# Kernel tuning notes

Measured on AMD Instinct MI355X. Metric: run time of the kernel, lower is better.

Reference implementation:

```python
import jax, jax.numpy as jnp
import numpy as np

D = 1024
H = 16
HD = D // H
FF = 4 * D
EPS = 1e-5


def setup_inputs() -> dict:
    key = jax.random.key(0)
    ks = jax.random.split(key, 16)
    s = lambda k, shape, scale: jax.random.normal(k, shape, dtype=jnp.float32) * scale
    inp = {
        "x": s(ks[0], (8, 1024, D), 1.0),
        "Wq": s(ks[1], (D, D), D ** -0.5), "bq": jnp.zeros((D,), jnp.float32),
        "Wk": s(ks[2], (D, D), D ** -0.5), "bk": jnp.zeros((D,), jnp.float32),
        "Wv": s(ks[3], (D, D), D ** -0.5), "bv": jnp.zeros((D,), jnp.float32),
        "Wo": s(ks[4], (D, D), D ** -0.5), "bo": jnp.zeros((D,), jnp.float32),
        "W1": s(ks[5], (D, FF), D ** -0.5), "b1": jnp.zeros((FF,), jnp.float32),
        "W2": s(ks[6], (FF, D), FF ** -0.5), "b2": jnp.zeros((D,), jnp.float32),
        "g1": jnp.ones((D,), jnp.float32), "be1": jnp.zeros((D,), jnp.float32),
        "g2": jnp.ones((D,), jnp.float32), "be2": jnp.zeros((D,), jnp.float32),
    }
    return inp


def _layernorm(x, g, b):
    mu = jnp.mean(x, axis=-1, keepdims=True)
    var = jnp.var(x, axis=-1, keepdims=True)
    return (x - mu) * jax.lax.rsqrt(var + EPS) * g + b


def reference(x, Wq, bq, Wk, bk, Wv, bv, Wo, bo, W1, b1, W2, b2, g1, be1, g2, be2):
    B, S, _ = x.shape
    # --- pre-norm attention block (dropout = identity in eval) ---
    h = _layernorm(x, g1, be1)
    q = (h @ Wq + bq).reshape(B, S, H, HD)
    k = (h @ Wk + bk).reshape(B, S, H, HD)
    v = (h @ Wv + bv).reshape(B, S, H, HD)
    scores = jnp.einsum('bqhd,bkhd->bhqk', q, k) / jnp.sqrt(jnp.float32(HD))
    attn = jax.nn.softmax(scores, axis=-1)
    ctx = jnp.einsum('bhqk,bkhd->bqhd', attn, v).reshape(B, S, D)
    x = x + (ctx @ Wo + bo)
    # --- pre-norm FFN block ---
    h = _layernorm(x, g2, be2)
    h = jax.nn.gelu(h @ W1 + b1, approximate=False)
    x = x + (h @ W2 + b2)
    return x
```

## Files before the change

### kernel.cpp

```cpp
#include <hip/hip_runtime.h>
#include <hip/hip_bf16.h>
#include <math.h>
#include <stdint.h>

typedef unsigned short u16;
typedef unsigned int u32;
typedef __attribute__((ext_vector_type(8))) short short8;
typedef __attribute__((ext_vector_type(4))) float f32x4;

__device__ __forceinline__ float b2f(u16 u) {
  union { u32 i; float f; } v; v.i = ((u32)u) << 16; return v.f;
}
__device__ __forceinline__ u16 f2b(float f) {
  union { float f; u32 i; } v; v.f = f;
  return (u16)((v.i + 0x7FFFu + ((v.i >> 16) & 1u)) >> 16);
}

__device__ __forceinline__ void gload_lds16(const u16* g, u16* l) {
  __builtin_amdgcn_global_load_lds((const __attribute__((address_space(1))) void*)g,
                                   (__attribute__((address_space(3))) void*)l, 16, 0, 0);
}

__global__ __launch_bounds__(256) void transpose_k(const float* __restrict__ in,
                                                   u16* __restrict__ out, int K, int N) {
  __shared__ u16 tile[32][33];
  int n0 = blockIdx.x * 32, k0 = blockIdx.y * 32;
  int tx = threadIdx.x & 31, ty = threadIdx.x >> 5;
  #pragma unroll
  for (int i = ty; i < 32; i += 8)
    tile[i][tx] = f2b(in[(size_t)(k0 + i) * N + n0 + tx]);
  __syncthreads();
  #pragma unroll
  for (int i = ty; i < 32; i += 8)
    out[(size_t)(n0 + i) * K + k0 + tx] = tile[tx][i];
}

__global__ __launch_bounds__(256) void cat3_k(const float* __restrict__ a, const float* __restrict__ b,
                                              const float* __restrict__ c, float* __restrict__ o) {
  int i = blockIdx.x * 256 + threadIdx.x;
  o[i] = i < 1024 ? a[i] : (i < 2048 ? b[i - 1024] : c[i - 2048]);
}

__global__ __launch_bounds__(256) void vtrans_k(const u16* __restrict__ qkv, u16* __restrict__ vt) {
  __shared__ u16 tile[32][33];
  int bh = blockIdx.y, b = bh >> 4, h = bh & 15;
  int s0 = (blockIdx.x & 31) * 32, d0 = (blockIdx.x >> 5) * 32;
  int tx = threadIdx.x & 31, ty = threadIdx.x >> 5;
  #pragma unroll
  for (int i = ty; i < 32; i += 8)
    tile[i][tx] = qkv[(size_t)(b * 1024 + s0 + i) * 3072 + 2048 + h * 64 + d0 + tx];
  __syncthreads();
  #pragma unroll
  for (int i = ty; i < 32; i += 8)
    vt[(size_t)(bh * 64 + d0 + i) * 1024 + s0 + tx] = tile[tx][i];
}

template<int FP32IN>
__global__ __launch_bounds__(256) void ln_k(const void* __restrict__ xv, const float* __restrict__ g,
                                            const float* __restrict__ be, u16* __restrict__ out) {
  int row = blockIdx.x, t = threadIdx.x;
  float f0, f1, f2, f3;
  if (FP32IN) {
    const float* xr = (const float*)xv + (size_t)row * 1024;
    float4 x4 = *(const float4*)(xr + t * 4);
    f0 = x4.x; f1 = x4.y; f2 = x4.z; f3 = x4.w;
  } else {
    const u16* xr = (const u16*)xv + (size_t)row * 1024;
    ushort4 x4 = *(const ushort4*)(xr + t * 4);
    f0 = b2f(x4.x); f1 = b2f(x4.y); f2 = b2f(x4.z); f3 = b2f(x4.w);
  }
  float s = f0 + f1 + f2 + f3;
  float ss = f0 * f0 + f1 * f1 + f2 * f2 + f3 * f3;
  #pragma unroll
  for (int off = 32; off > 0; off >>= 1) { s += __shfl_down(s, off); ss += __shfl_down(ss, off); }
  __shared__ float sb[4], ssb[4];
  if ((t & 63) == 0) { sb[t >> 6] = s; ssb[t >> 6] = ss; }
  __syncthreads();
  s = sb[0] + sb[1] + sb[2] + sb[3];
  ss = ssb[0] + ssb[1] + ssb[2] + ssb[3];
  float mu = s * (1.0f / 1024.0f);
  float var = ss * (1.0f / 1024.0f) - mu * mu;
  float rstd = rsqrtf(var + 1e-5f);
  float4 gv = *(const float4*)(g + t * 4);
  float4 bv = *(const float4*)(be + t * 4);
  ushort4 o;
  o.x = f2b((f0 - mu) * rstd * gv.x + bv.x);
  o.y = f2b((f1 - mu) * rstd * gv.y + bv.y);
  o.z = f2b((f2 - mu) * rstd * gv.z + bv.z);
  o.w = f2b((f3 - mu) * rstd * gv.w + bv.w);
  *(ushort4*)(out + (size_t)row * 1024 + t * 4) = o;
}

template<int ACT, int RESID, int OUTF32>
__global__ __launch_bounds__(256) void gemm_k(const u16* __restrict__ A, const u16* __restrict__ Bt,
                                              const float* __restrict__ bias, const void* __restrict__ resid,
                                              void* __restrict__ Cv, int M, int N, int K, int ldc) {
  __shared__ u16 As[2][128 * 32];
  __shared__ u16 Bs[2][128 * 32];
  int Ny = N >> 7;
  int lin = blockIdx.y * 64 + blockIdx.x;
  int c8 = lin & 7, sblk = lin >> 3;
  int mq = sblk / Ny;
  int m0 = ((mq << 3) | c8) << 7;
  int n0 = (sblk - mq * Ny) << 7;
  int t = threadIdx.x;
  int wave = t >> 6, lane = t & 63, quad = lane >> 4, l16 = lane & 15;
  int wm = (wave >> 1) * 64, wn = (wave & 1) * 64;
  f32x4 acc[4][4] = {};
  int lr = lane >> 2;
  int lc = (lane & 3) ^ (lr & 3);
  const u16* Ab = A + (size_t)(m0 + wave * 16 + lr) * K + lc * 8;
  const u16* Bb = Bt + (size_t)(n0 + wave * 16 + lr) * K + lc * 8;
  const int lb = wave * 16 * 32;
  const int rdoff = (quad ^ (l16 & 3)) * 8;
  #pragma unroll
  for (int i = 0; i < 2; i++) {
    gload_lds16(Ab + (size_t)i * 64 * K, &As[0][lb + i * 64 * 32]);
    gload_lds16(Bb + (size_t)i * 64 * K, &Bs[0][lb + i * 64 * 32]);
  }
  const int niter = K >> 5;
  for (int c = 0; c < niter; c++) {
    int buf = c & 1;
    __syncthreads();
    if (c + 1 < niter) {
      int k1 = (c + 1) << 5;
      #pragma unroll
      for (int i = 0; i < 2; i++) {
        gload_lds16(Ab + k1 + (size_t)i * 64 * K, &As[buf ^ 1][lb + i * 64 * 32]);
        gload_lds16(Bb + k1 + (size_t)i * 64 * K, &Bs[buf ^ 1][lb + i * 64 * 32]);
      }
    }
    short8 a[4], b[4];
    #pragma unroll
    for (int i = 0; i < 4; i++)
      a[i] = *(const short8*)(&As[buf][(wm + i * 16 + l16) * 32 + rdoff]);
    #pragma unroll
    for (int j = 0; j < 4; j++)
      b[j] = *(const short8*)(&Bs[buf][(wn + j * 16 + l16) * 32 + rdoff]);
    #pragma unroll
    for (int i = 0; i < 4; i++)
      #pragma unroll
      for (int j = 0; j < 4; j++)
        acc[i][j] = __builtin_amdgcn_mfma_f32_16x16x32_bf16(a[i], b[j], acc[i][j], 0, 0, 0);
  }
  float bcol[4];
  #pragma unroll
  for (int j = 0; j < 4; j++) bcol[j] = bias[n0 + wn + j * 16 + l16];
  #pragma unroll
  for (int i = 0; i < 4; i++) {
    #pragma unroll
    for (int r = 0; r < 4; r++) {
      int row = m0 + wm + i * 16 + quad * 4 + r;
      #pragma unroll
      for (int j = 0; j < 4; j++) {
        int col = n0 + wn + j * 16 + l16;
        float v = acc[i][j][r] + bcol[j];
        if (ACT == 1) {
          float e = v * (2.3022082f + 0.1029431f * v * v);
          float tt = exp2f(fminf(e, 80.0f));
          v = v * tt / (tt + 1.0f);
        }
        if (RESID == 1) v += b2f(((const u16*)resid)[(size_t)row * N + col]);
        if (RESID == 2) v += ((const float*)resid)[(size_t)row * N + col];
        if (OUTF32) ((float*)Cv)[(size_t)row * ldc + col] = v;
        else        ((u16*)Cv)[(size_t)row * ldc + col] = f2b(v);
      }
    }
  }
}

__global__ __launch_bounds__(256) void attn_k(const u16* __restrict__ QKV, const u16* __restrict__ VT,
                                              u16* __restrict__ ctx) {
  int bh = blockIdx.x;
  int b = bh >> 4;
  int q0 = blockIdx.y * 64;
  int t = threadIdx.x, wave = t >> 6, lane = t & 63, quad = lane >> 4, l16 = lane & 15;
  __shared__ u16 Ks[2][64 * 64];
  __shared__ u16 Vs[2][64 * 64];
  __shared__ u16 Plds[4][16][72];
  const size_t base = ((size_t)b * 1024) * 3072 + (size_t)(bh & 15) * 64;
  const u16* Kbase = QKV + base + 1024;
  const u16* vtb = VT + (size_t)bh * 64 * 1024;
  int lrow = lane >> 3;
  int lchunk = (lane & 7) ^ (lrow & 7);
  int srow = wave * 16;
  short8 qa[2];
  #pragma unroll
  for (int kh = 0; kh < 2; kh++)
    qa[kh] = *(const short8*)(QKV + base + (size_t)(q0 + wave * 16 + l16) * 3072 + kh * 32 + quad * 8);
  #pragma unroll
  for (int half = 0; half < 2; half++) {
    int r8 = srow + half * 8;
    gload_lds16(Kbase + (size_t)(r8 + lrow) * 3072 + lchunk * 8, &Ks[0][r8 * 64]);
    gload_lds16(vtb + (size_t)(r8 + lrow) * 1024 + lchunk * 8, &Vs[0][r8 * 64]);
  }
  f32x4 o[4] = {};
  float l_acc[4] = {0.f, 0.f, 0.f, 0.f};
  for (int c = 0; c < 16; c++) {
    int buf = c & 1;
    __syncthreads();
    if (c < 15) {
      #pragma unroll
      for (int half = 0; half < 2; half++) {
        int r8 = srow + half * 8;
        gload_lds16(Kbase + (size_t)((c + 1) * 64 + r8 + lrow) * 3072 + lchunk * 8, &Ks[buf ^ 1][r8 * 64]);
        gload_lds16(vtb + (size_t)(r8 + lrow) * 1024 + (c + 1) * 64 + lchunk * 8, &Vs[buf ^ 1][r8 * 64]);
      }
    }
    f32x4 s[4] = {};
    #pragma unroll
    for (int kh = 0; kh < 2; kh++)
      #pragma unroll
      for (int j = 0; j < 4; j++) {
        int row = j * 16 + l16;
        int pc = (kh * 4 + quad) ^ (row & 7);
        short8 kb = *(const short8*)(&Ks[buf][row * 64 + pc * 8]);
        s[j] = __builtin_amdgcn_mfma_f32_16x16x32_bf16(qa[kh], kb, s[j], 0, 0, 0);
      }
    #pragma unroll
    for (int j = 0; j < 4; j++)
      #pragma unroll
      for (int r = 0; r < 4; r++) {
        float p = exp2f(s[j][r] * 0.18033688011112042f);
        l_acc[r] += p;
        Plds[wave][quad * 4 + r][j * 16 + l16] = f2b(p);
      }
    #pragma unroll
    for (int kh = 0; kh < 2; kh++) {
      short8 pa = *(const short8*)(&Plds[wave][l16][kh * 32 + quad * 8]);
      #pragma unroll
      for (int d4 = 0; d4 < 4; d4++) {
        int row = d4 * 16 + l16;
        int pc = (kh * 4 + quad) ^ (row & 7);
        short8 vb = *(const short8*)(&Vs[buf][row * 64 + pc * 8]);
        o[d4] = __builtin_amdgcn_mfma_f32_16x16x32_bf16(pa, vb, o[d4], 0, 0, 0);
      }
    }
  }
  #pragma unroll
  for (int off = 1; off < 16; off <<= 1)
    #pragma unroll
    for (int r = 0; r < 4; r++) l_acc[r] += __shfl_xor(l_acc[r], off);
  #pragma unroll
  for (int r = 0; r < 4; r++) {
    float inv = 1.0f / l_acc[r];
    size_t row = (size_t)b * 1024 + q0 + wave * 16 + quad * 4 + r;
    #pragma unroll
    for (int d4 = 0; d4 < 4; d4++) {
      int col = (bh & 15) * 64 + d4 * 16 + l16;
      ctx[row * 1024 + col] = f2b(o[d4][r] * inv);
    }
  }
}

extern "C" void kernel_launch(void* const* d_in, const int* in_sizes, int n_in,
                              void* d_out, int out_size, void* d_ws, size_t ws_size,
                              hipStream_t stream) {
  const float* x   = (const float*)d_in[0];
  const float* Wq  = (const float*)d_in[1];  const float* bq  = (const float*)d_in[2];
  const float* Wk  = (const float*)d_in[3];  const float* bk  = (const float*)d_in[4];
  const float* Wv  = (const float*)d_in[5];  const float* bv  = (const float*)d_in[6];
  const float* Wo  = (const float*)d_in[7];  const float* bo  = (const float*)d_in[8];
  const float* W1  = (const float*)d_in[9];  const float* b1  = (const float*)d_in[10];
  const float* W2  = (const float*)d_in[11]; const float* b2  = (const float*)d_in[12];
  const float* g1  = (const float*)d_in[13]; const float* be1 = (const float*)d_in[14];
  const float* g2  = (const float*)d_in[15]; const float* be2 = (const float*)d_in[16];

  char* ws = (char*)d_ws;
  const size_t MB = 1024 * 1024;
  u16* h1    = (u16*)(ws + 0 * MB);
  u16* qkv   = (u16*)(ws + 16 * MB);
  u16* x1    = (u16*)(ws + 16 * MB);
  u16* h2    = (u16*)(ws + 32 * MB);
  u16* W2T   = (u16*)(ws + 48 * MB);
  u16* WqkvT = (u16*)(ws + 64 * MB);
  u16* WoT   = (u16*)(ws + 70 * MB);
  u16* W1T   = (u16*)(ws + 72 * MB);
  float* bqkv = (float*)(ws + 80 * MB);
  u16* h3f   = (u16*)(ws + 80 * MB);
  u16* vt    = h1;
  u16* ctx   = (u16*)d_out;
  float* out = (float*)d_out;

  transpose_k<<<dim3(32, 32), 256, 0, stream>>>(Wq, WqkvT, 1024, 1024);
  transpose_k<<<dim3(32, 32), 256, 0, stream>>>(Wk, WqkvT + (size_t)1024 * 1024, 1024, 1024);
  transpose_k<<<dim3(32, 32), 256, 0, stream>>>(Wv, WqkvT + (size_t)2048 * 1024, 1024, 1024);
  transpose_k<<<dim3(32, 32), 256, 0, stream>>>(Wo, WoT, 1024, 1024);
  transpose_k<<<dim3(128, 32), 256, 0, stream>>>(W1, W1T, 1024, 4096);
  cat3_k<<<12, 256, 0, stream>>>(bq, bk, bv, bqkv);

  ln_k<1><<<8192, 256, 0, stream>>>(x, g1, be1, h1);

  gemm_k<0, 0, 0><<<dim3(64, 24), 256, 0, stream>>>(h1, WqkvT, bqkv, nullptr, qkv,
                                                    8192, 3072, 1024, 3072);

  vtrans_k<<<dim3(64, 128), 256, 0, stream>>>(qkv, vt);

  attn_k<<<dim3(128, 16), 256, 0, stream>>>(qkv, vt, ctx);

  gemm_k<0, 2, 0><<<dim3(64, 8), 256, 0, stream>>>(ctx, WoT, bo, x, x1,
                                                   8192, 1024, 1024, 1024);

  transpose_k<<<dim3(32, 128), 256, 0, stream>>>(W2, W2T, 4096, 1024);

  ln_k<0><<<8192, 256, 0, stream>>>(x1, g2, be2, h2);

  gemm_k<1, 0, 0><<<dim3(64, 32), 256, 0, stream>>>(h2, W1T, b1, nullptr, h3f,
                                                    8192, 4096, 1024, 4096);
  gemm_k<0, 1, 1><<<dim3(64, 8), 256, 0, stream>>>(h3f, W2T, b2, x1, out,
                                                   8192, 1024, 4096, 1024);

  (void)in_sizes; (void)n_in; (void)out_size; (void)ws_size;
}
```

Baseline: 545.1 us.

## Triple-buffer GEMM LDS tiles with two-stage prefetch and manual waitcnt barriers

Changes the GEMM main loop from double to triple buffering in LDS, prefetching two K-tiles ahead. It replaces __syncthreads with explicit vmcnt waits plus s_barrier, so loads for later tiles can stay in flight across the barrier. It also raises wave priority around the MFMA block. This costs 50% more LDS per block, which may reduce occupancy, and it relies on the manual waitcnt counts being correct.

```diff
diff --git a/kernel.cpp b/kernel.cpp
--- a/kernel.cpp
+++ b/kernel.cpp
@@ -95,8 +95,8 @@
 __global__ __launch_bounds__(256) void gemm_k(const u16* __restrict__ A, const u16* __restrict__ Bt,
                                               const float* __restrict__ bias, const void* __restrict__ resid,
                                               void* __restrict__ Cv, int M, int N, int K, int ldc) {
-  __shared__ u16 As[2][128 * 32];
-  __shared__ u16 Bs[2][128 * 32];
+  __shared__ u16 As[3][128 * 32];
+  __shared__ u16 Bs[3][128 * 32];
   int Ny = N >> 7;
   int lin = blockIdx.y * 64 + blockIdx.x;
   int c8 = lin & 7, sblk = lin >> 3;
@@ -113,21 +113,29 @@
   const u16* Bb = Bt + (size_t)(n0 + wave * 16 + lr) * K + lc * 8;
   const int lb = wave * 16 * 32;
   const int rdoff = (quad ^ (l16 & 3)) * 8;
+  const int niter = K >> 5;
   #pragma unroll
   for (int i = 0; i < 2; i++) {
     gload_lds16(Ab + (size_t)i * 64 * K, &As[0][lb + i * 64 * 32]);
     gload_lds16(Bb + (size_t)i * 64 * K, &Bs[0][lb + i * 64 * 32]);
   }
-  const int niter = K >> 5;
+  #pragma unroll
+  for (int i = 0; i < 2; i++) {
+    gload_lds16(Ab + 32 + (size_t)i * 64 * K, &As[1][lb + i * 64 * 32]);
+    gload_lds16(Bb + 32 + (size_t)i * 64 * K, &Bs[1][lb + i * 64 * 32]);
+  }
+  asm volatile("s_waitcnt vmcnt(4)" ::: "memory");
+  __builtin_amdgcn_s_barrier();
+  __builtin_amdgcn_sched_barrier(0);
+  int buf = 0;
   for (int c = 0; c < niter; c++) {
-    int buf = c & 1;
-    __syncthreads();
-    if (c + 1 < niter) {
-      int k1 = (c + 1) << 5;
+    if (c + 2 < niter) {
+      int k2 = (c + 2) << 5;
+      int wb = buf + 2; if (wb >= 3) wb -= 3;
       #pragma unroll
       for (int i = 0; i < 2; i++) {
-        gload_lds16(Ab + k1 + (size_t)i * 64 * K, &As[buf ^ 1][lb + i * 64 * 32]);
-        gload_lds16(Bb + k1 + (size_t)i * 64 * K, &Bs[buf ^ 1][lb + i * 64 * 32]);
+        gload_lds16(Ab + k2 + (size_t)i * 64 * K, &As[wb][lb + i * 64 * 32]);
+        gload_lds16(Bb + k2 + (size_t)i * 64 * K, &Bs[wb][lb + i * 64 * 32]);
       }
     }
     short8 a[4], b[4];
@@ -137,11 +145,23 @@
     #pragma unroll
     for (int j = 0; j < 4; j++)
       b[j] = *(const short8*)(&Bs[buf][(wn + j * 16 + l16) * 32 + rdoff]);
+    __builtin_amdgcn_s_setprio(1);
     #pragma unroll
     for (int i = 0; i < 4; i++)
       #pragma unroll
       for (int j = 0; j < 4; j++)
         acc[i][j] = __builtin_amdgcn_mfma_f32_16x16x32_bf16(a[i], b[j], acc[i][j], 0, 0, 0);
+    __builtin_amdgcn_s_setprio(0);
+    if (c + 2 < niter) {
+      asm volatile("s_waitcnt vmcnt(4)" ::: "memory");
+    } else if (c + 1 < niter) {
+      asm volatile("s_waitcnt vmcnt(0)" ::: "memory");
+    }
+    if (c + 1 < niter) {
+      __builtin_amdgcn_s_barrier();
+      __builtin_amdgcn_sched_barrier(0);
+    }
+    buf = (buf == 2) ? 0 : buf + 1;
   }
   float bcol[4];
   #pragma unroll
```

New measurement: 554.8 us. About the same (+1.8%).

## Rewrite GEMM as 128x256 tile, 8 waves, triple-buffered K=64 pipeline

Applied to the files above, without the earlier changes.

The GEMM kernel moves from a 128x128 tile with 4 waves and double-buffered K=32 stages to a 128x256 tile with 8 waves and triple-buffered K=64 stages. Global-to-LDS prefetch is interleaved with the MFMA phases and guarded by explicit barriers, waitcnts and setprio. The aim is to hide load latency, raise arithmetic intensity per block and cut synchronisation per unit of K. The costs are more LDS (about 144KB) and fewer blocks, so occupancy drops and tail imbalance grows.

```diff
diff --git a/kernel.cpp b/kernel.cpp
--- a/kernel.cpp
+++ b/kernel.cpp
@@ -20,6 +20,9 @@
   __builtin_amdgcn_global_load_lds((const __attribute__((address_space(1))) void*)g,
                                    (__attribute__((address_space(3))) void*)l, 16, 0, 0);
 }
+
+#define LD8(p) (*(const short8*)(p))
+#define MFMA_BF16 __builtin_amdgcn_mfma_f32_16x16x32_bf16
 
 __global__ __launch_bounds__(256) void transpose_k(const float* __restrict__ in,
                                                    u16* __restrict__ out, int K, int N) {
@@ -92,56 +95,149 @@
 }
 
 template<int ACT, int RESID, int OUTF32>
-__global__ __launch_bounds__(256) void gemm_k(const u16* __restrict__ A, const u16* __restrict__ Bt,
+__global__ __launch_bounds__(512) void gemm_k(const u16* __restrict__ A, const u16* __restrict__ Bt,
                                               const float* __restrict__ bias, const void* __restrict__ resid,
                                               void* __restrict__ Cv, int M, int N, int K, int ldc) {
-  __shared__ u16 As[2][128 * 32];
-  __shared__ u16 Bs[2][128 * 32];
-  int Ny = N >> 7;
+  __shared__ u16 As[3][128 * 64];
+  __shared__ u16 Bs[3][256 * 64];
+  int Ny = N >> 8;
   int lin = blockIdx.y * 64 + blockIdx.x;
   int c8 = lin & 7, sblk = lin >> 3;
   int mq = sblk / Ny;
   int m0 = ((mq << 3) | c8) << 7;
-  int n0 = (sblk - mq * Ny) << 7;
+  int n0 = (sblk - mq * Ny) << 8;
   int t = threadIdx.x;
   int wave = t >> 6, lane = t & 63, quad = lane >> 4, l16 = lane & 15;
-  int wm = (wave >> 1) * 64, wn = (wave & 1) * 64;
+  int wm = (wave >> 2) << 6;
+  int wn = (wave & 3) << 6;
   f32x4 acc[4][4] = {};
-  int lr = lane >> 2;
-  int lc = (lane & 3) ^ (lr & 3);
-  const u16* Ab = A + (size_t)(m0 + wave * 16 + lr) * K + lc * 8;
-  const u16* Bb = Bt + (size_t)(n0 + wave * 16 + lr) * K + lc * 8;
-  const int lb = wave * 16 * 32;
-  const int rdoff = (quad ^ (l16 & 3)) * 8;
-  #pragma unroll
-  for (int i = 0; i < 2; i++) {
-    gload_lds16(Ab + (size_t)i * 64 * K, &As[0][lb + i * 64 * 32]);
-    gload_lds16(Bb + (size_t)i * 64 * K, &Bs[0][lb + i * 64 * 32]);
-  }
-  const int niter = K >> 5;
-  for (int c = 0; c < niter; c++) {
-    int buf = c & 1;
-    __syncthreads();
-    if (c + 1 < niter) {
-      int k1 = (c + 1) << 5;
-      #pragma unroll
-      for (int i = 0; i < 2; i++) {
-        gload_lds16(Ab + k1 + (size_t)i * 64 * K, &As[buf ^ 1][lb + i * 64 * 32]);
-        gload_lds16(Bb + k1 + (size_t)i * 64 * K, &Bs[buf ^ 1][lb + i * 64 * 32]);
-      }
-    }
-    short8 a[4], b[4];
-    #pragma unroll
-    for (int i = 0; i < 4; i++)
-      a[i] = *(const short8*)(&As[buf][(wm + i * 16 + l16) * 32 + rdoff]);
-    #pragma unroll
-    for (int j = 0; j < 4; j++)
-      b[j] = *(const short8*)(&Bs[buf][(wn + j * 16 + l16) * 32 + rdoff]);
-    #pragma unroll
-    for (int i = 0; i < 4; i++)
-      #pragma unroll
-      for (int j = 0; j < 4; j++)
-        acc[i][j] = __builtin_amdgcn_mfma_f32_16x16x32_bf16(a[i], b[j], acc[i][j], 0, 0, 0);
+  int lrow = lane >> 3;
+  int lchunk = (lane & 7) ^ lrow;
+  const u16* Ab = A + (size_t)(m0 + wave * 16 + lrow) * K + lchunk * 8;
+  const u16* Bb = Bt + (size_t)(n0 + wave * 32 + lrow) * K + lchunk * 8;
+  const int aw = wave * 16 * 64;
+  const int bw = wave * 32 * 64;
+  const int x7 = l16 & 7;
+  const int rbA = (wm + l16) * 64;
+  const int rbB = (wn + l16) * 64;
+  const int c0 = (quad ^ x7) * 8;
+  const int c1 = ((4 + quad) ^ x7) * 8;
+  const int niter = K >> 6;
+  #pragma unroll
+  for (int g = 0; g < 2; g++) gload_lds16(Ab + (size_t)g * 8 * K, &As[0][aw + g * 8 * 64]);
+  #pragma unroll
+  for (int g = 0; g < 4; g++) gload_lds16(Bb + (size_t)g * 8 * K, &Bs[0][bw + g * 8 * 64]);
+  #pragma unroll
+  for (int g = 0; g < 2; g++) gload_lds16(Ab + 64 + (size_t)g * 8 * K, &As[1][aw + g * 8 * 64]);
+  #pragma unroll
+  for (int g = 0; g < 4; g++) gload_lds16(Bb + 64 + (size_t)g * 8 * K, &Bs[1][bw + g * 8 * 64]);
+  asm volatile("s_waitcnt vmcnt(6)" ::: "memory");
+  __builtin_amdgcn_s_barrier();
+  __builtin_amdgcn_sched_barrier(0);
+  int cur = 0;
+  for (int tt = 0; tt < niter; tt++) {
+    const u16* Ac = &As[cur][0];
+    const u16* Bc = &Bs[cur][0];
+    int wb = cur + 2; if (wb >= 3) wb -= 3;
+    const bool pf = (tt + 2 < niter);
+    const int kpf = (tt + 2) << 6;
+    short8 a0, a1, a2, a3, b0, b1, b2, b3;
+    a0 = LD8(Ac + rbA + c0);
+    a1 = LD8(Ac + rbA + 1024 + c0);
+    b0 = LD8(Bc + rbB + c0);
+    b1 = LD8(Bc + rbB + 1024 + c0);
+    b2 = LD8(Bc + rbB + 2048 + c0);
+    b3 = LD8(Bc + rbB + 3072 + c0);
+    if (pf) {
+      gload_lds16(Ab + kpf, &As[wb][aw]);
+      gload_lds16(Ab + kpf + (size_t)8 * K, &As[wb][aw + 8 * 64]);
+    }
+    __builtin_amdgcn_s_barrier();
+    asm volatile("s_waitcnt lgkmcnt(0)" ::: "memory");
+    __builtin_amdgcn_sched_barrier(0);
+    __builtin_amdgcn_s_setprio(1);
+    acc[0][0] = MFMA_BF16(a0, b0, acc[0][0], 0, 0, 0);
+    acc[0][1] = MFMA_BF16(a0, b1, acc[0][1], 0, 0, 0);
+    acc[0][2] = MFMA_BF16(a0, b2, acc[0][2], 0, 0, 0);
+    acc[0][3] = MFMA_BF16(a0, b3, acc[0][3], 0, 0, 0);
+    acc[1][0] = MFMA_BF16(a1, b0, acc[1][0], 0, 0, 0);
+    acc[1][1] = MFMA_BF16(a1, b1, acc[1][1], 0, 0, 0);
+    acc[1][2] = MFMA_BF16(a1, b2, acc[1][2], 0, 0, 0);
+    acc[1][3] = MFMA_BF16(a1, b3, acc[1][3], 0, 0, 0);
+    __builtin_amdgcn_s_setprio(0);
+    __builtin_amdgcn_s_barrier();
+    __builtin_amdgcn_sched_barrier(0);
+    a2 = LD8(Ac + rbA + 2048 + c0);
+    a3 = LD8(Ac + rbA + 3072 + c0);
+    if (pf) {
+      gload_lds16(Bb + kpf, &Bs[wb][bw]);
+      gload_lds16(Bb + kpf + (size_t)8 * K, &Bs[wb][bw + 8 * 64]);
+    }
+    __builtin_amdgcn_s_barrier();
+    asm volatile("s_waitcnt lgkmcnt(0)" ::: "memory");
+    __builtin_amdgcn_sched_barrier(0);
+    __builtin_amdgcn_s_setprio(1);
+    acc[2][0] = MFMA_BF16(a2, b0, acc[2][0], 0, 0, 0);
+    acc[2][1] = MFMA_BF16(a2, b1, acc[2][1], 0, 0, 0);
+    acc[2][2] = MFMA_BF16(a2, b2, acc[2][2], 0, 0, 0);
+    acc[2][3] = MFMA_BF16(a2, b3, acc[2][3], 0, 0, 0);
+    acc[3][0] = MFMA_BF16(a3, b0, acc[3][0], 0, 0, 0);
+    acc[3][1] = MFMA_BF16(a3, b1, acc[3][1], 0, 0, 0);
+    acc[3][2] = MFMA_BF16(a3, b2, acc[3][2], 0, 0, 0);
+    acc[3][3] = MFMA_BF16(a3, b3, acc[3][3], 0, 0, 0);
+    __builtin_amdgcn_s_setprio(0);
+    __builtin_amdgcn_s_barrier();
+    __builtin_amdgcn_sched_barrier(0);
+    a0 = LD8(Ac + rbA + c1);
+    a1 = LD8(Ac + rbA + 1024 + c1);
+    b0 = LD8(Bc + rbB + c1);
+    b1 = LD8(Bc + rbB + 1024 + c1);
+    b2 = LD8(Bc + rbB + 2048 + c1);
+    b3 = LD8(Bc + rbB + 3072 + c1);
+    if (pf) {
+      gload_lds16(Bb + kpf + (size_t)16 * K, &Bs[wb][bw + 16 * 64]);
+      gload_lds16(Bb + kpf + (size_t)24 * K, &Bs[wb][bw + 24 * 64]);
+    }
+    __builtin_amdgcn_s_barrier();
+    asm volatile("s_waitcnt lgkmcnt(0)" ::: "memory");
+    __builtin_amdgcn_sched_barrier(0);
+    __builtin_amdgcn_s_setprio(1);
+    acc[0][0] = MFMA_BF16(a0, b0, acc[0][0], 0, 0, 0);
+    acc[0][1] = MFMA_BF16(a0, b1, acc[0][1], 0, 0, 0);
+    acc[0][2] = MFMA_BF16(a0, b2, acc[0][2], 0, 0, 0);
+    acc[0][3] = MFMA_BF16(a0, b3, acc[0][3], 0, 0, 0);
+    acc[1][0] = MFMA_BF16(a1, b0, acc[1][0], 0, 0, 0);
+    acc[1][1] = MFMA_BF16(a1, b1, acc[1][1], 0, 0, 0);
+    acc[1][2] = MFMA_BF16(a1, b2, acc[1][2], 0, 0, 0);
+    acc[1][3] = MFMA_BF16(a1, b3, acc[1][3], 0, 0, 0);
+    __builtin_amdgcn_s_setprio(0);
+    __builtin_amdgcn_s_barrier();
+    __builtin_amdgcn_sched_barrier(0);
+    a2 = LD8(Ac + rbA + 2048 + c1);
+    a3 = LD8(Ac + rbA + 3072 + c1);
+    __builtin_amdgcn_s_barrier();
+    asm volatile("s_waitcnt lgkmcnt(0)" ::: "memory");
+    __builtin_amdgcn_sched_barrier(0);
+    __builtin_amdgcn_s_setprio(1);
+    acc[2][0] = MFMA_BF16(a2, b0, acc[2][0], 0, 0, 0);
+    acc[2][1] = MFMA_BF16(a2, b1, acc[2][1], 0, 0, 0);
+    acc[2][2] = MFMA_BF16(a2, b2, acc[2][2], 0, 0, 0);
+    acc[2][3] = MFMA_BF16(a2, b3, acc[2][3], 0, 0, 0);
+    acc[3][0] = MFMA_BF16(a3, b0, acc[3][0], 0, 0, 0);
+    acc[3][1] = MFMA_BF16(a3, b1, acc[3][1], 0, 0, 0);
+    acc[3][2] = MFMA_BF16(a3, b2, acc[3][2], 0, 0, 0);
+    acc[3][3] = MFMA_BF16(a3, b3, acc[3][3], 0, 0, 0);
+    __builtin_amdgcn_s_setprio(0);
+    if (tt + 2 < niter) {
+      asm volatile("s_waitcnt vmcnt(6)" ::: "memory");
+    } else if (tt + 1 < niter) {
+      asm volatile("s_waitcnt vmcnt(0)" ::: "memory");
+    }
+    if (tt + 1 < niter) {
+      __builtin_amdgcn_s_barrier();
+      __builtin_amdgcn_sched_barrier(0);
+    }
+    cur = (cur == 2) ? 0 : cur + 1;
   }
   float bcol[4];
   #pragma unroll
@@ -157,8 +253,8 @@
         float v = acc[i][j][r] + bcol[j];
         if (ACT == 1) {
           float e = v * (2.3022082f + 0.1029431f * v * v);
-          float tt = exp2f(fminf(e, 80.0f));
-          v = v * tt / (tt + 1.0f);
+          float tt2 = exp2f(fminf(e, 80.0f));
+          v = v * tt2 / (tt2 + 1.0f);
         }
         if (RESID == 1) v += b2f(((const u16*)resid)[(size_t)row * N + col]);
         if (RESID == 2) v += ((const float*)resid)[(size_t)row * N + col];
@@ -291,23 +387,23 @@
 
   ln_k<1><<<8192, 256, 0, stream>>>(x, g1, be1, h1);
 
-  gemm_k<0, 0, 0><<<dim3(64, 24), 256, 0, stream>>>(h1, WqkvT, bqkv, nullptr, qkv,
+  gemm_k<0, 0, 0><<<dim3(64, 12), 512, 0, stream>>>(h1, WqkvT, bqkv, nullptr, qkv,
                                                     8192, 3072, 1024, 3072);
 
   vtrans_k<<<dim3(64, 128), 256, 0, stream>>>(qkv, vt);
 
   attn_k<<<dim3(128, 16), 256, 0, stream>>>(qkv, vt, ctx);
 
-  gemm_k<0, 2, 0><<<dim3(64, 8), 256, 0, stream>>>(ctx, WoT, bo, x, x1,
+  gemm_k<0, 2, 0><<<dim3(64, 4), 512, 0, stream>>>(ctx, WoT, bo, x, x1,
                                                    8192, 1024, 1024, 1024);
 
   transpose_k<<<dim3(32, 128), 256, 0, stream>>>(W2, W2T, 4096, 1024);
 
   ln_k<0><<<8192, 256, 0, stream>>>(x1, g2, be2, h2);
 
-  gemm_k<1, 0, 0><<<dim3(64, 32), 256, 0, stream>>>(h2, W1T, b1, nullptr, h3f,
+  gemm_k<1, 0, 0><<<dim3(64, 16), 512, 0, stream>>>(h2, W1T, b1, nullptr, h3f,
                                                     8192, 4096, 1024, 4096);
-  gemm_k<0, 1, 1><<<dim3(64, 8), 256, 0, stream>>>(h3f, W2T, b2, x1, out,
+  gemm_k<0, 1, 1><<<dim3(64, 4), 512, 0, stream>>>(h3f, W2T, b2, x1, out,
                                                    8192, 1024, 4096, 1024);
 
   (void)in_sizes; (void)n_in; (void)out_size; (void)ws_size;
```

Result: slower. 567.6 us (+4.1%).

## Add 256x256 tiled GEMM with 4-stage LDS pipeline for QKV and FFN1

Applied to the files above, without the earlier changes.

Adds a new GEMM kernel with 256x256 output tiles, 512 threads (8 waves, each computing 128x64), and a 4-buffer LDS ring fed by global_load_lds prefetch three steps ahead. Inside each K step it interleaves the LDS fragment reads, split prefetches and MFMA bursts using explicit barriers, waitcnt and setprio. The QKV and FFN-up GEMMs use it to get more data reuse per loaded byte and to hide memory latency. It also changes the LDS swizzle in the existing GEMM. The costs are higher LDS use per block (128 KB), more register pressure and fewer blocks in the grid.

```diff
diff --git a/kernel.cpp b/kernel.cpp
--- a/kernel.cpp
+++ b/kernel.cpp
@@ -20,6 +20,9 @@
   __builtin_amdgcn_global_load_lds((const __attribute__((address_space(1))) void*)g,
                                    (__attribute__((address_space(3))) void*)l, 16, 0, 0);
 }
+
+#define LD8(p) (*(const short8*)(p))
+#define MFMA_BF16 __builtin_amdgcn_mfma_f32_16x16x32_bf16
 
 __global__ __launch_bounds__(256) void transpose_k(const float* __restrict__ in,
                                                    u16* __restrict__ out, int K, int N) {
@@ -108,11 +111,11 @@
   int wm = (wave >> 1) * 64, wn = (wave & 1) * 64;
   f32x4 acc[4][4] = {};
   int lr = lane >> 2;
-  int lc = (lane & 3) ^ (lr & 3);
+  int lc = (lane & 3) ^ ((lane >> 4) & 3);
   const u16* Ab = A + (size_t)(m0 + wave * 16 + lr) * K + lc * 8;
   const u16* Bb = Bt + (size_t)(n0 + wave * 16 + lr) * K + lc * 8;
   const int lb = wave * 16 * 32;
-  const int rdoff = (quad ^ (l16 & 3)) * 8;
+  const int rdoff = (quad ^ ((l16 >> 2) & 3)) * 8;
   #pragma unroll
   for (int i = 0; i < 2; i++) {
     gload_lds16(Ab + (size_t)i * 64 * K, &As[0][lb + i * 64 * 32]);
@@ -133,15 +136,15 @@
     short8 a[4], b[4];
     #pragma unroll
     for (int i = 0; i < 4; i++)
-      a[i] = *(const short8*)(&As[buf][(wm + i * 16 + l16) * 32 + rdoff]);
+      a[i] = LD8(&As[buf][(wm + i * 16 + l16) * 32 + rdoff]);
     #pragma unroll
     for (int j = 0; j < 4; j++)
-      b[j] = *(const short8*)(&Bs[buf][(wn + j * 16 + l16) * 32 + rdoff]);
+      b[j] = LD8(&Bs[buf][(wn + j * 16 + l16) * 32 + rdoff]);
     #pragma unroll
     for (int i = 0; i < 4; i++)
       #pragma unroll
       for (int j = 0; j < 4; j++)
-        acc[i][j] = __builtin_amdgcn_mfma_f32_16x16x32_bf16(a[i], b[j], acc[i][j], 0, 0, 0);
+        acc[i][j] = MFMA_BF16(a[i], b[j], acc[i][j], 0, 0, 0);
   }
   float bcol[4];
   #pragma unroll
@@ -159,6 +162,130 @@
           float e = v * (2.3022082f + 0.1029431f * v * v);
           float tt = exp2f(fminf(e, 80.0f));
           v = v * tt / (tt + 1.0f);
+        }
+        if (RESID == 1) v += b2f(((const u16*)resid)[(size_t)row * N + col]);
+        if (RESID == 2) v += ((const float*)resid)[(size_t)row * N + col];
+        if (OUTF32) ((float*)Cv)[(size_t)row * ldc + col] = v;
+        else        ((u16*)Cv)[(size_t)row * ldc + col] = f2b(v);
+      }
+    }
+  }
+}
+
+template<int ACT, int RESID, int OUTF32>
+__global__ __launch_bounds__(512, 2) void gemm256_k(const u16* __restrict__ A, const u16* __restrict__ Bt,
+                                                    const float* __restrict__ bias, const void* __restrict__ resid,
+                                                    void* __restrict__ Cv, int M, int N, int K, int ldc) {
+  __shared__ u16 As[4][256 * 32];
+  __shared__ u16 Bs[4][256 * 32];
+  int Ny = N >> 8;
+  int lin = blockIdx.y * 32 + blockIdx.x;
+  int c8 = lin & 7, sblk = lin >> 3;
+  int mq = sblk / Ny;
+  int m0 = ((mq << 3) | c8) << 8;
+  int n0 = (sblk - mq * Ny) << 8;
+  int t = threadIdx.x;
+  int wave = t >> 6, lane = t & 63, quad = lane >> 4, l16 = lane & 15;
+  int wm = (wave >> 2) << 7;
+  int wn = (wave & 3) << 6;
+  f32x4 acc[8][4] = {};
+  int lr = lane >> 2;
+  int lc = (lane & 3) ^ ((lane >> 4) & 3);
+  const u16* Ab = A + (size_t)(m0 + wave * 16 + lr) * K + lc * 8;
+  const u16* Bb = Bt + (size_t)(n0 + wave * 16 + lr) * K + lc * 8;
+  const int lbA = wave * 16 * 32;
+  const int cswz = (quad ^ ((l16 >> 2) & 3)) * 8;
+  const int rdA = (wm + l16) * 32 + cswz;
+  const int rdB = (wn + l16) * 32 + cswz;
+  const int niter = K >> 5;
+  #pragma unroll
+  for (int p = 0; p < 3; p++) {
+    #pragma unroll
+    for (int g = 0; g < 2; g++) {
+      gload_lds16(Ab + (p << 5) + (size_t)g * 128 * K, &As[p][lbA + g * 128 * 32]);
+      gload_lds16(Bb + (p << 5) + (size_t)g * 128 * K, &Bs[p][lbA + g * 128 * 32]);
+    }
+  }
+  asm volatile("s_waitcnt vmcnt(8)" ::: "memory");
+  __builtin_amdgcn_s_barrier();
+  __builtin_amdgcn_sched_barrier(0);
+  for (int tt = 0; tt < niter; tt++) {
+    int buf = tt & 3, wb = (tt + 3) & 3;
+    const bool pf = (tt + 3 < niter);
+    const int kpf = (tt + 3) << 5;
+    const u16* Ac = &As[buf][0];
+    const u16* Bc = &Bs[buf][0];
+    short8 a[8], b[4];
+    a[0] = LD8(Ac + rdA);
+    a[1] = LD8(Ac + rdA + 512);
+    a[2] = LD8(Ac + rdA + 1024);
+    a[3] = LD8(Ac + rdA + 1536);
+    b[0] = LD8(Bc + rdB);
+    b[1] = LD8(Bc + rdB + 512);
+    b[2] = LD8(Bc + rdB + 1024);
+    b[3] = LD8(Bc + rdB + 1536);
+    if (pf) {
+      gload_lds16(Ab + kpf, &As[wb][lbA]);
+      gload_lds16(Ab + kpf + (size_t)128 * K, &As[wb][lbA + 128 * 32]);
+    }
+    __builtin_amdgcn_s_barrier();
+    asm volatile("s_waitcnt lgkmcnt(0)" ::: "memory");
+    __builtin_amdgcn_sched_barrier(0);
+    __builtin_amdgcn_s_setprio(1);
+    #pragma unroll
+    for (int i = 0; i < 4; i++)
+      #pragma unroll
+      for (int j = 0; j < 4; j++)
+        acc[i][j] = MFMA_BF16(a[i], b[j], acc[i][j], 0, 0, 0);
+    __builtin_amdgcn_s_setprio(0);
+    __builtin_amdgcn_s_barrier();
+    __builtin_amdgcn_sched_barrier(0);
+    a[4] = LD8(Ac + rdA + 2048);
+    a[5] = LD8(Ac + rdA + 2560);
+    a[6] = LD8(Ac + rdA + 3072);
+    a[7] = LD8(Ac + rdA + 3584);
+    if (pf) {
+      gload_lds16(Bb + kpf, &Bs[wb][lbA]);
+      gload_lds16(Bb + kpf + (size_t)128 * K, &Bs[wb][lbA + 128 * 32]);
+    }
+    __builtin_amdgcn_s_barrier();
+    asm volatile("s_waitcnt lgkmcnt(0)" ::: "memory");
+    __builtin_amdgcn_sched_barrier(0);
+    __builtin_amdgcn_s_setprio(1);
+    #pragma unroll
+    for (int i = 4; i < 8; i++)
+      #pragma unroll
+      for (int j = 0; j < 4; j++)
+        acc[i][j] = MFMA_BF16(a[i], b[j], acc[i][j], 0, 0, 0);
+    __builtin_amdgcn_s_setprio(0);
+    if (tt + 3 < niter) {
+      asm volatile("s_waitcnt vmcnt(8)" ::: "memory");
+    } else if (tt + 2 < niter) {
+      asm volatile("s_waitcnt vmcnt(4)" ::: "memory");
+    } else if (tt + 1 < niter) {
+      asm volatile("s_waitcnt vmcnt(0)" ::: "memory");
+    }
+    if (tt + 1 < niter) {
+      __builtin_amdgcn_s_barrier();
+      __builtin_amdgcn_sched_barrier(0);
+    }
+  }
+  float bcol[4];
+  #pragma unroll
+  for (int j = 0; j < 4; j++) bcol[j] = bias[n0 + wn + j * 16 + l16];
+  #pragma unroll
+  for (int i = 0; i < 8; i++) {
+    #pragma unroll
+    for (int r = 0; r < 4; r++) {
+      int row = m0 + wm + i * 16 + quad * 4 + r;
+      #pragma unroll
+      for (int j = 0; j < 4; j++) {
+        int col = n0 + wn + j * 16 + l16;
+        float v = acc[i][j][r] + bcol[j];
+        if (ACT == 1) {
+          float e = v * (2.3022082f + 0.1029431f * v * v);
+          float tt2 = exp2f(fminf(e, 80.0f));
+          v = v * tt2 / (tt2 + 1.0f);
         }
         if (RESID == 1) v += b2f(((const u16*)resid)[(size_t)row * N + col]);
         if (RESID == 2) v += ((const float*)resid)[(size_t)row * N + col];
@@ -215,7 +342,7 @@
         int row = j * 16 + l16;
         int pc = (kh * 4 + quad) ^ (row & 7);
         short8 kb = *(const short8*)(&Ks[buf][row * 64 + pc * 8]);
-        s[j] = __builtin_amdgcn_mfma_f32_16x16x32_bf16(qa[kh], kb, s[j], 0, 0, 0);
+        s[j] = MFMA_BF16(qa[kh], kb, s[j], 0, 0, 0);
       }
     #pragma unroll
     for (int j = 0; j < 4; j++)
@@ -233,7 +360,7 @@
         int row = d4 * 16 + l16;
         int pc = (kh * 4 + quad) ^ (row & 7);
         short8 vb = *(const short8*)(&Vs[buf][row * 64 + pc * 8]);
-        o[d4] = __builtin_amdgcn_mfma_f32_16x16x32_bf16(pa, vb, o[d4], 0, 0, 0);
+        o[d4] = MFMA_BF16(pa, vb, o[d4], 0, 0, 0);
       }
     }
   }
@@ -291,8 +418,8 @@
 
   ln_k<1><<<8192, 256, 0, stream>>>(x, g1, be1, h1);
 
-  gemm_k<0, 0, 0><<<dim3(64, 24), 256, 0, stream>>>(h1, WqkvT, bqkv, nullptr, qkv,
-                                                    8192, 3072, 1024, 3072);
+  gemm256_k<0, 0, 0><<<dim3(32, 12), 512, 0, stream>>>(h1, WqkvT, bqkv, nullptr, qkv,
+                                                       8192, 3072, 1024, 3072);
 
   vtrans_k<<<dim3(64, 128), 256, 0, stream>>>(qkv, vt);
 
@@ -305,8 +432,8 @@
 
   ln_k<0><<<8192, 256, 0, stream>>>(x1, g2, be2, h2);
 
-  gemm_k<1, 0, 0><<<dim3(64, 32), 256, 0, stream>>>(h2, W1T, b1, nullptr, h3f,
-                                                    8192, 4096, 1024, 4096);
+  gemm256_k<1, 0, 0><<<dim3(32, 16), 512, 0, stream>>>(h2, W1T, b1, nullptr, h3f,
+                                                       8192, 4096, 1024, 4096);
   gemm_k<0, 1, 1><<<dim3(64, 8), 256, 0, stream>>>(h3f, W2T, b2, x1, out,
                                                    8192, 1024, 4096, 1024);
 
```

New measurement: 546.6 us. Within noise of the previous version (+0.3%).
